# Kernel optimization log

Hardware: AMD Instinct MI355X
Metric: run time of the kernel (lower is better)

## Reference

```python
import jax, jax.numpy as jnp
import numpy as np
import math

B, S, QD, KD, LD, H = 32, 8192, 256, 256, 256, 8
SD = LD // H  # split_dim = 32

def setup_inputs() -> dict:
    key = jax.random.key(0)
    ks = jax.random.split(key, 8)
    query = jax.random.normal(ks[0], (B, QD), dtype=jnp.float32)
    keys = jax.random.normal(ks[1], (B, S, KD), dtype=jnp.float32)
    # binary padding mask: 1 = keep, 0 = pad
    padding_mask = (jax.random.uniform(ks[2], (B, 1, 1, S)) > 0.1).astype(jnp.float32)
    s = 1.0 / math.sqrt(KD)
    Wq = jax.random.normal(ks[3], (LD, QD), dtype=jnp.float32) * s
    Wk = jax.random.normal(ks[4], (LD, KD), dtype=jnp.float32) * s
    Wv = jax.random.normal(ks[5], (LD, KD), dtype=jnp.float32) * s
    Wu = jax.random.normal(ks[6], (LD, LD), dtype=jnp.float32) * (1.0 / math.sqrt(LD))
    bu = jnp.zeros((LD,), dtype=jnp.float32)
    return {"query": query, "keys": keys, "padding_mask": padding_mask,
            "Wq": Wq, "Wk": Wk, "Wv": Wv, "Wu": Wu, "bu": bu}

def reference(query, keys, padding_mask, Wq, Wk, Wv, Wu, bu):
    attn_mask_penalty = -10000.0
    b, s, _ = keys.shape
    # projections (torch Linear: x @ W.T)
    q = query @ Wq.T                      # (b, LD)
    k = keys @ Wk.T                       # (b, s, LD)
    v = keys @ Wv.T                       # (b, s, LD)
    q = q.reshape(b, H, SD)               # single query per head
    k = k.reshape(b, s, H, SD)
    v = v.reshape(b, s, H, SD)
    # scores: (b, H, 1, s)
    dot = jnp.einsum('bhd,bshd->bhs', q, k) / math.sqrt(SD)
    dot = dot[:, :, None, :]              # (b, H, 1, s)
    unmasked = dot
    masked = dot + (1.0 - padding_mask) * attn_mask_penalty
    attn = jax.nn.softmax(masked, axis=-1)  # (b, H, 1, s)
    out = jnp.einsum('bhs,bshd->bhd', attn[:, :, 0, :], v)  # (b, H, SD)
    out = out.reshape(b, H * SD)
    unified = out @ Wu.T + bu             # (b, LD)
    return (unified, unmasked)
```

## Files before the change

### kernel.cpp

```cpp
#include <hip/hip_runtime.h>

#define B_   32
#define S_   8192
#define C_   256
#define LD_  256
#define H_   8
#define SD_  32
#define CH   64
#define NCH  (S_ / CH)

#define WS_QK    0
#define WS_LSUM  (WS_QK + B_*H_*C_)
#define WS_CTX   (WS_LSUM + B_*H_)
#define WS_TOTAL (WS_CTX + B_*H_*C_)

__global__ __launch_bounds__(256) void proj_qk(const float* __restrict__ query,
                                               const float* __restrict__ Wq,
                                               const float* __restrict__ Wk,
                                               float* __restrict__ ws) {
    const int b = blockIdx.x, t = threadIdx.x;
    __shared__ float qry[C_];
    __shared__ float qv[LD_];
    qry[t] = query[b * C_ + t];
    __syncthreads();
    {
        const float* wr = Wq + t * C_;
        float a = 0.f;
        for (int c = 0; c < C_; c += 4) {
            float4 w = *(const float4*)(wr + c);
            float4 x = *(const float4*)(qry + c);
            a = fmaf(w.x, x.x, fmaf(w.y, x.y, fmaf(w.z, x.z, fmaf(w.w, x.w, a))));
        }
        qv[t] = a;
    }
    __syncthreads();
    const float scale = 0.17677669529663687f;
    float* qkb = ws + WS_QK + b * H_ * C_;
    #pragma unroll
    for (int h = 0; h < H_; h++) {
        float a = 0.f;
        #pragma unroll 8
        for (int d = 0; d < SD_; d++) {
            a = fmaf(qv[h * SD_ + d], Wk[(h * SD_ + d) * C_ + t], a);
        }
        qkb[h * C_ + t] = a * scale;
    }
}

__global__ __launch_bounds__(256) void attn_pass(const float* __restrict__ keys,
                                                 const float* __restrict__ pmask,
                                                 const float* __restrict__ ws_qk,
                                                 float* __restrict__ lsum,
                                                 float* __restrict__ ctxsum,
                                                 float* __restrict__ out_unmasked) {
    const int b = blockIdx.y, ch = blockIdx.x, t = threadIdx.x;
    const int s0 = ch * CH;
    __shared__ float qk_s[H_][C_];
    __shared__ float part[4][H_][CH];
    __shared__ float p_t[CH][H_];
    __shared__ float pm_s[CH];

    {
        const float4* src = (const float4*)(ws_qk + b * H_ * C_);
        float4* dst = (float4*)&qk_s[0][0];
        dst[t]       = src[t];
        dst[t + 256] = src[t + 256];
    }
    if (t < CH) pm_s[t] = __builtin_nontemporal_load(pmask + b * S_ + s0 + t);
    __syncthreads();

    {
        const int sl = t & 63, q = t >> 6;
        const float* krow = keys + ((size_t)b * S_ + s0 + sl) * C_ + q * 64;
        const float* qrow = &qk_s[0][q * 64];
        float acc0 = 0.f, acc1 = 0.f, acc2 = 0.f, acc3 = 0.f;
        float acc4 = 0.f, acc5 = 0.f, acc6 = 0.f, acc7 = 0.f;
        #pragma unroll
        for (int c = 0; c < 64; c += 4) {
            float4 kv = *(const float4*)(krow + c);
            float4 w0 = *(const float4*)(qrow + 0 * C_ + c);
            float4 w1 = *(const float4*)(qrow + 1 * C_ + c);
            float4 w2 = *(const float4*)(qrow + 2 * C_ + c);
            float4 w3 = *(const float4*)(qrow + 3 * C_ + c);
            float4 w4 = *(const float4*)(qrow + 4 * C_ + c);
            float4 w5 = *(const float4*)(qrow + 5 * C_ + c);
            float4 w6 = *(const float4*)(qrow + 6 * C_ + c);
            float4 w7 = *(const float4*)(qrow + 7 * C_ + c);
            acc0 = fmaf(kv.x, w0.x, fmaf(kv.y, w0.y, fmaf(kv.z, w0.z, fmaf(kv.w, w0.w, acc0))));
            acc1 = fmaf(kv.x, w1.x, fmaf(kv.y, w1.y, fmaf(kv.z, w1.z, fmaf(kv.w, w1.w, acc1))));
            acc2 = fmaf(kv.x, w2.x, fmaf(kv.y, w2.y, fmaf(kv.z, w2.z, fmaf(kv.w, w2.w, acc2))));
            acc3 = fmaf(kv.x, w3.x, fmaf(kv.y, w3.y, fmaf(kv.z, w3.z, fmaf(kv.w, w3.w, acc3))));
            acc4 = fmaf(kv.x, w4.x, fmaf(kv.y, w4.y, fmaf(kv.z, w4.z, fmaf(kv.w, w4.w, acc4))));
            acc5 = fmaf(kv.x, w5.x, fmaf(kv.y, w5.y, fmaf(kv.z, w5.z, fmaf(kv.w, w5.w, acc5))));
            acc6 = fmaf(kv.x, w6.x, fmaf(kv.y, w6.y, fmaf(kv.z, w6.z, fmaf(kv.w, w6.w, acc6))));
            acc7 = fmaf(kv.x, w7.x, fmaf(kv.y, w7.y, fmaf(kv.z, w7.z, fmaf(kv.w, w7.w, acc7))));
        }
        part[q][0][sl] = acc0; part[q][1][sl] = acc1;
        part[q][2][sl] = acc2; part[q][3][sl] = acc3;
        part[q][4][sl] = acc4; part[q][5][sl] = acc5;
        part[q][6][sl] = acc6; part[q][7][sl] = acc7;
    }
    __syncthreads();

    {
        const int s = t & 63, g = t >> 6;
        const int h0 = 2 * g, h1 = 2 * g + 1;
        const float pen = (1.0f - pm_s[s]) * -10000.0f;
        float d0 = part[0][h0][s] + part[1][h0][s] + part[2][h0][s] + part[3][h0][s];
        float d1 = part[0][h1][s] + part[1][h1][s] + part[2][h1][s] + part[3][h1][s];
        float* ub = out_unmasked + (size_t)(b * H_) * S_ + s0 + s;
        __builtin_nontemporal_store(d0, ub + (size_t)h0 * S_);
        __builtin_nontemporal_store(d1, ub + (size_t)h1 * S_);
        float p0 = __expf(d0 + pen);
        float p1 = __expf(d1 + pen);
        p_t[s][h0] = p0;
        p_t[s][h1] = p1;
        float r0 = p0, r1 = p1;
        #pragma unroll
        for (int off = 32; off > 0; off >>= 1) {
            r0 += __shfl_xor(r0, off);
            r1 += __shfl_xor(r1, off);
        }
        if (s == 0) {
            atomicAdd(&lsum[b * H_ + h0], r0);
            atomicAdd(&lsum[b * H_ + h1], r1);
        }
    }
    __syncthreads();

    {
        float f0 = 0.f, f1 = 0.f, f2 = 0.f, f3 = 0.f;
        float f4 = 0.f, f5 = 0.f, f6 = 0.f, f7 = 0.f;
        const float* kcol = keys + ((size_t)b * S_ + s0) * C_ + t;
        #pragma unroll 4
        for (int s = 0; s < CH; ++s) {
            float kv = kcol[(size_t)s * C_];
            float4 pA = *(const float4*)&p_t[s][0];
            float4 pB = *(const float4*)&p_t[s][4];
            f0 = fmaf(pA.x, kv, f0); f1 = fmaf(pA.y, kv, f1);
            f2 = fmaf(pA.z, kv, f2); f3 = fmaf(pA.w, kv, f3);
            f4 = fmaf(pB.x, kv, f4); f5 = fmaf(pB.y, kv, f5);
            f6 = fmaf(pB.z, kv, f6); f7 = fmaf(pB.w, kv, f7);
        }
        float* cb = ctxsum + (size_t)b * H_ * C_ + t;
        atomicAdd(cb + 0 * C_, f0); atomicAdd(cb + 1 * C_, f1);
        atomicAdd(cb + 2 * C_, f2); atomicAdd(cb + 3 * C_, f3);
        atomicAdd(cb + 4 * C_, f4); atomicAdd(cb + 5 * C_, f5);
        atomicAdd(cb + 6 * C_, f6); atomicAdd(cb + 7 * C_, f7);
    }
}

__global__ __launch_bounds__(256) void finalize(const float* __restrict__ Wv,
                                                const float* __restrict__ Wu,
                                                const float* __restrict__ bu,
                                                const float* __restrict__ lsum,
                                                const float* __restrict__ ctxsum,
                                                float* __restrict__ out_unified) {
    const int b = blockIdx.x, t = threadIdx.x;
    __shared__ float ctxn[H_ * C_];
    __shared__ float outv[LD_];
    __shared__ float linv[H_];
    if (t < H_) linv[t] = 1.0f / lsum[b * H_ + t];
    __syncthreads();
    for (int i = t; i < H_ * C_; i += 256)
        ctxn[i] = ctxsum[(size_t)b * H_ * C_ + i] * linv[i >> 8];
    __syncthreads();
    {
        const float* wr = Wv + t * C_;
        const float* cx = ctxn + (t >> 5) * C_;
        float a = 0.f;
        for (int c = 0; c < C_; c += 4) {
            float4 w = *(const float4*)(wr + c);
            float4 x = *(const float4*)(cx + c);
            a = fmaf(w.x, x.x, fmaf(w.y, x.y, fmaf(w.z, x.z, fmaf(w.w, x.w, a))));
        }
        outv[t] = a;
    }
    __syncthreads();
    {
        const float* wr = Wu + t * C_;
        float a = bu[t];
        for (int c = 0; c < C_; c += 4) {
            float4 w = *(const float4*)(wr + c);
            float4 x = *(const float4*)(outv + c);
            a = fmaf(w.x, x.x, fmaf(w.y, x.y, fmaf(w.z, x.z, fmaf(w.w, x.w, a))));
        }
        out_unified[b * LD_ + t] = a;
    }
}

extern "C" void kernel_launch(void* const* d_in, const int* in_sizes, int n_in,
                              void* d_out, int out_size, void* d_ws, size_t ws_size,
                              hipStream_t stream) {
    const float* query = (const float*)d_in[0];
    const float* keys  = (const float*)d_in[1];
    const float* pmask = (const float*)d_in[2];
    const float* Wq    = (const float*)d_in[3];
    const float* Wk    = (const float*)d_in[4];
    const float* Wv    = (const float*)d_in[5];
    const float* Wu    = (const float*)d_in[6];
    const float* bu    = (const float*)d_in[7];

    float* out          = (float*)d_out;
    float* out_unified  = out;
    float* out_unmasked = out + B_ * LD_;
    float* ws           = (float*)d_ws;

    hipMemsetAsync(ws + WS_LSUM, 0, (size_t)(B_ * H_ + B_ * H_ * C_) * sizeof(float), stream);

    proj_qk<<<B_, 256, 0, stream>>>(query, Wq, Wk, ws);

    dim3 gridB(NCH, B_);
    attn_pass<<<gridB, 256, 0, stream>>>(keys, pmask, ws + WS_QK,
                                         ws + WS_LSUM, ws + WS_CTX, out_unmasked);

    finalize<<<B_, 256, 0, stream>>>(Wv, Wu, bu, ws + WS_LSUM, ws + WS_CTX, out_unified);
}
```

Baseline: 541.9 us.

## Make attention blocks persistent with an LDS key tile and register context accumulators

The attention pass now launches 32 blocks per batch. Each block loops over strided 32-row chunks, stages every key chunk once into a padded LDS tile, and reuses that tile for both the score and the context phases instead of reading keys from global memory twice. Context and softmax-denominator partials stay in registers across chunks and are flushed with one set of atomics per block, which removes the per-chunk atomic traffic. In exchange the kernel adds an extra barrier per chunk, has a serial loop per block, and uses more LDS, which may limit occupancy.

```diff
diff --git a/kernel.cpp b/kernel.cpp
--- a/kernel.cpp
+++ b/kernel.cpp
@@ -6,13 +6,14 @@
 #define LD_  256
 #define H_   8
 #define SD_  32
-#define CH   64
-#define NCH  (S_ / CH)
+#define CH   32
+#define NCHUNK (S_ / CH)
+#define BPB  32
+#define CPB  (NCHUNK / BPB)
 
 #define WS_QK    0
 #define WS_LSUM  (WS_QK + B_*H_*C_)
 #define WS_CTX   (WS_LSUM + B_*H_)
-#define WS_TOTAL (WS_CTX + B_*H_*C_)
 
 __global__ __launch_bounds__(256) void proj_qk(const float* __restrict__ query,
                                                const float* __restrict__ Wq,
@@ -47,106 +48,128 @@
     }
 }
 
-__global__ __launch_bounds__(256) void attn_pass(const float* __restrict__ keys,
-                                                 const float* __restrict__ pmask,
-                                                 const float* __restrict__ ws_qk,
-                                                 float* __restrict__ lsum,
-                                                 float* __restrict__ ctxsum,
-                                                 float* __restrict__ out_unmasked) {
-    const int b = blockIdx.y, ch = blockIdx.x, t = threadIdx.x;
-    const int s0 = ch * CH;
-    __shared__ float qk_s[H_][C_];
-    __shared__ float part[4][H_][CH];
-    __shared__ float p_t[CH][H_];
-    __shared__ float pm_s[CH];
+__global__ __launch_bounds__(256, 2) void attn_pass(const float* __restrict__ keys,
+                                                    const float* __restrict__ pmask,
+                                                    const float* __restrict__ ws_qk,
+                                                    float* __restrict__ lsum,
+                                                    float* __restrict__ ctxsum,
+                                                    float* __restrict__ out_unmasked) {
+    const int b = blockIdx.x >> 5, bp = blockIdx.x & 31, t = threadIdx.x;
+    __shared__ float2 tile2[CH][129];
+    __shared__ float  qk_s[H_ * C_];
+    __shared__ float  part[8][H_][CH];
+    __shared__ float  p_t[CH][H_];
 
     {
         const float4* src = (const float4*)(ws_qk + b * H_ * C_);
-        float4* dst = (float4*)&qk_s[0][0];
+        float4* dst = (float4*)qk_s;
         dst[t]       = src[t];
         dst[t + 256] = src[t + 256];
     }
-    if (t < CH) pm_s[t] = __builtin_nontemporal_load(pmask + b * S_ + s0 + t);
-    __syncthreads();
-
-    {
-        const int sl = t & 63, q = t >> 6;
-        const float* krow = keys + ((size_t)b * S_ + s0 + sl) * C_ + q * 64;
-        const float* qrow = &qk_s[0][q * 64];
-        float acc0 = 0.f, acc1 = 0.f, acc2 = 0.f, acc3 = 0.f;
-        float acc4 = 0.f, acc5 = 0.f, acc6 = 0.f, acc7 = 0.f;
+
+    float ctx_acc[H_][2];
+    #pragma unroll
+    for (int h = 0; h < H_; h++) { ctx_acc[h][0] = 0.f; ctx_acc[h][1] = 0.f; }
+    float lsum_reg = 0.f;
+
+    const int st_row = t >> 3, st_j = t & 7;
+    const int p1_sl = t & 31, p1_q = t >> 5;
+    const int rd_s = t & 31, rd_g = t >> 5;
+    const int p3_c2 = t & 127, p3_sg = t >> 7;
+
+    for (int i = 0; i < CPB; i++) {
+        const int s0 = (bp + BPB * i) * CH;
+        __syncthreads();
+
+        {
+            const float4* g = (const float4*)(keys + ((size_t)b * S_ + s0 + st_row) * C_);
+            #pragma unroll
+            for (int k = 0; k < 8; k++) {
+                const int f4 = st_j + 8 * k;
+                float4 v = g[f4];
+                tile2[st_row][2 * f4]     = make_float2(v.x, v.y);
+                tile2[st_row][2 * f4 + 1] = make_float2(v.z, v.w);
+            }
+        }
+        __syncthreads();
+
+        {
+            float2 kvr[16];
+            const float2* kr = &tile2[p1_sl][p1_q * 16];
+            #pragma unroll
+            for (int j = 0; j < 16; j++) kvr[j] = kr[j];
+            #pragma unroll
+            for (int h = 0; h < H_; h++) {
+                float a = 0.f;
+                #pragma unroll
+                for (int c4 = 0; c4 < 8; c4++) {
+                    float4 qv = *(const float4*)(qk_s + h * C_ + p1_q * 32 + 4 * c4);
+                    a = fmaf(kvr[2*c4].x, qv.x, fmaf(kvr[2*c4].y, qv.y,
+                        fmaf(kvr[2*c4+1].x, qv.z, fmaf(kvr[2*c4+1].y, qv.w, a))));
+                }
+                part[p1_q][h][p1_sl] = a;
+            }
+        }
+        __syncthreads();
+
+        {
+            const float pm = pmask[b * S_ + s0 + rd_s];
+            float d = 0.f;
+            #pragma unroll
+            for (int q = 0; q < 8; q++) d += part[q][rd_g][rd_s];
+            __builtin_nontemporal_store(d, out_unmasked + ((size_t)b * H_ + rd_g) * S_ + s0 + rd_s);
+            const float pen = (1.0f - pm) * -10000.0f;
+            float p = __expf(d + pen);
+            p_t[rd_s][rd_g] = p;
+            lsum_reg += p;
+        }
+        __syncthreads();
+
+        {
+            const int sbase = p3_sg * 16;
+            #pragma unroll
+            for (int si = 0; si < 16; si++) {
+                const int s = sbase + si;
+                float2 kv = tile2[s][p3_c2];
+                float4 pA = *(const float4*)&p_t[s][0];
+                float4 pB = *(const float4*)&p_t[s][4];
+                ctx_acc[0][0] = fmaf(pA.x, kv.x, ctx_acc[0][0]); ctx_acc[0][1] = fmaf(pA.x, kv.y, ctx_acc[0][1]);
+                ctx_acc[1][0] = fmaf(pA.y, kv.x, ctx_acc[1][0]); ctx_acc[1][1] = fmaf(pA.y, kv.y, ctx_acc[1][1]);
+                ctx_acc[2][0] = fmaf(pA.z, kv.x, ctx_acc[2][0]); ctx_acc[2][1] = fmaf(pA.z, kv.y, ctx_acc[2][1]);
+                ctx_acc[3][0] = fmaf(pA.w, kv.x, ctx_acc[3][0]); ctx_acc[3][1] = fmaf(pA.w, kv.y, ctx_acc[3][1]);
+                ctx_acc[4][0] = fmaf(pB.x, kv.x, ctx_acc[4][0]); ctx_acc[4][1] = fmaf(pB.x, kv.y, ctx_acc[4][1]);
+                ctx_acc[5][0] = fmaf(pB.y, kv.x, ctx_acc[5][0]); ctx_acc[5][1] = fmaf(pB.y, kv.y, ctx_acc[5][1]);
+                ctx_acc[6][0] = fmaf(pB.z, kv.x, ctx_acc[6][0]); ctx_acc[6][1] = fmaf(pB.z, kv.y, ctx_acc[6][1]);
+                ctx_acc[7][0] = fmaf(pB.w, kv.x, ctx_acc[7][0]); ctx_acc[7][1] = fmaf(pB.w, kv.y, ctx_acc[7][1]);
+            }
+        }
+    }
+
+    __syncthreads();
+    {
+        float r = lsum_reg;
         #pragma unroll
-        for (int c = 0; c < 64; c += 4) {
-            float4 kv = *(const float4*)(krow + c);
-            float4 w0 = *(const float4*)(qrow + 0 * C_ + c);
-            float4 w1 = *(const float4*)(qrow + 1 * C_ + c);
-            float4 w2 = *(const float4*)(qrow + 2 * C_ + c);
-            float4 w3 = *(const float4*)(qrow + 3 * C_ + c);
-            float4 w4 = *(const float4*)(qrow + 4 * C_ + c);
-            float4 w5 = *(const float4*)(qrow + 5 * C_ + c);
-            float4 w6 = *(const float4*)(qrow + 6 * C_ + c);
-            float4 w7 = *(const float4*)(qrow + 7 * C_ + c);
-            acc0 = fmaf(kv.x, w0.x, fmaf(kv.y, w0.y, fmaf(kv.z, w0.z, fmaf(kv.w, w0.w, acc0))));
-            acc1 = fmaf(kv.x, w1.x, fmaf(kv.y, w1.y, fmaf(kv.z, w1.z, fmaf(kv.w, w1.w, acc1))));
-            acc2 = fmaf(kv.x, w2.x, fmaf(kv.y, w2.y, fmaf(kv.z, w2.z, fmaf(kv.w, w2.w, acc2))));
-            acc3 = fmaf(kv.x, w3.x, fmaf(kv.y, w3.y, fmaf(kv.z, w3.z, fmaf(kv.w, w3.w, acc3))));
-            acc4 = fmaf(kv.x, w4.x, fmaf(kv.y, w4.y, fmaf(kv.z, w4.z, fmaf(kv.w, w4.w, acc4))));
-            acc5 = fmaf(kv.x, w5.x, fmaf(kv.y, w5.y, fmaf(kv.z, w5.z, fmaf(kv.w, w5.w, acc5))));
-            acc6 = fmaf(kv.x, w6.x, fmaf(kv.y, w6.y, fmaf(kv.z, w6.z, fmaf(kv.w, w6.w, acc6))));
-            acc7 = fmaf(kv.x, w7.x, fmaf(kv.y, w7.y, fmaf(kv.z, w7.z, fmaf(kv.w, w7.w, acc7))));
-        }
-        part[q][0][sl] = acc0; part[q][1][sl] = acc1;
-        part[q][2][sl] = acc2; part[q][3][sl] = acc3;
-        part[q][4][sl] = acc4; part[q][5][sl] = acc5;
-        part[q][6][sl] = acc6; part[q][7][sl] = acc7;
-    }
-    __syncthreads();
-
-    {
-        const int s = t & 63, g = t >> 6;
-        const int h0 = 2 * g, h1 = 2 * g + 1;
-        const float pen = (1.0f - pm_s[s]) * -10000.0f;
-        float d0 = part[0][h0][s] + part[1][h0][s] + part[2][h0][s] + part[3][h0][s];
-        float d1 = part[0][h1][s] + part[1][h1][s] + part[2][h1][s] + part[3][h1][s];
-        float* ub = out_unmasked + (size_t)(b * H_) * S_ + s0 + s;
-        __builtin_nontemporal_store(d0, ub + (size_t)h0 * S_);
-        __builtin_nontemporal_store(d1, ub + (size_t)h1 * S_);
-        float p0 = __expf(d0 + pen);
-        float p1 = __expf(d1 + pen);
-        p_t[s][h0] = p0;
-        p_t[s][h1] = p1;
-        float r0 = p0, r1 = p1;
-        #pragma unroll
-        for (int off = 32; off > 0; off >>= 1) {
-            r0 += __shfl_xor(r0, off);
-            r1 += __shfl_xor(r1, off);
-        }
-        if (s == 0) {
-            atomicAdd(&lsum[b * H_ + h0], r0);
-            atomicAdd(&lsum[b * H_ + h1], r1);
-        }
-    }
-    __syncthreads();
-
-    {
-        float f0 = 0.f, f1 = 0.f, f2 = 0.f, f3 = 0.f;
-        float f4 = 0.f, f5 = 0.f, f6 = 0.f, f7 = 0.f;
-        const float* kcol = keys + ((size_t)b * S_ + s0) * C_ + t;
-        #pragma unroll 4
-        for (int s = 0; s < CH; ++s) {
-            float kv = kcol[(size_t)s * C_];
-            float4 pA = *(const float4*)&p_t[s][0];
-            float4 pB = *(const float4*)&p_t[s][4];
-            f0 = fmaf(pA.x, kv, f0); f1 = fmaf(pA.y, kv, f1);
-            f2 = fmaf(pA.z, kv, f2); f3 = fmaf(pA.w, kv, f3);
-            f4 = fmaf(pB.x, kv, f4); f5 = fmaf(pB.y, kv, f5);
-            f6 = fmaf(pB.z, kv, f6); f7 = fmaf(pB.w, kv, f7);
-        }
-        float* cb = ctxsum + (size_t)b * H_ * C_ + t;
-        atomicAdd(cb + 0 * C_, f0); atomicAdd(cb + 1 * C_, f1);
-        atomicAdd(cb + 2 * C_, f2); atomicAdd(cb + 3 * C_, f3);
-        atomicAdd(cb + 4 * C_, f4); atomicAdd(cb + 5 * C_, f5);
-        atomicAdd(cb + 6 * C_, f6); atomicAdd(cb + 7 * C_, f7);
+        for (int off = 16; off > 0; off >>= 1) r += __shfl_xor(r, off);
+        if (rd_s == 0) atomicAdd(&lsum[b * H_ + rd_g], r);
+    }
+    {
+        float* sc = &part[0][0][0];
+        if (p3_sg == 1) {
+            #pragma unroll
+            for (int h = 0; h < H_; h++) {
+                sc[h * C_ + 2 * p3_c2]     = ctx_acc[h][0];
+                sc[h * C_ + 2 * p3_c2 + 1] = ctx_acc[h][1];
+            }
+        }
+        __syncthreads();
+        if (p3_sg == 0) {
+            float* cb = ctxsum + (size_t)b * H_ * C_;
+            #pragma unroll
+            for (int h = 0; h < H_; h++) {
+                atomicAdd(&cb[h * C_ + 2 * p3_c2],     ctx_acc[h][0] + sc[h * C_ + 2 * p3_c2]);
+                atomicAdd(&cb[h * C_ + 2 * p3_c2 + 1], ctx_acc[h][1] + sc[h * C_ + 2 * p3_c2 + 1]);
+            }
+        }
     }
 }
 
@@ -210,9 +233,8 @@
 
     proj_qk<<<B_, 256, 0, stream>>>(query, Wq, Wk, ws);
 
-    dim3 gridB(NCH, B_);
-    attn_pass<<<gridB, 256, 0, stream>>>(keys, pmask, ws + WS_QK,
-                                         ws + WS_LSUM, ws + WS_CTX, out_unmasked);
+    attn_pass<<<B_ * BPB, 256, 0, stream>>>(keys, pmask, ws + WS_QK,
+                                            ws + WS_LSUM, ws + WS_CTX, out_unmasked);
 
     finalize<<<B_, 256, 0, stream>>>(Wv, Wu, bu, ws + WS_LSUM, ws + WS_CTX, out_unified);
 }
```

Measured after the change: 482.4 us. 1.12x faster.
